# Kernel optimization log

Measured on AMD Instinct MI355X. Metric: run time of the kernel, lower is better.

## Reference

```python
import jax, jax.numpy as jnp
import numpy as np

N, NFEAT, NHID, NCLASS, NLAYERS = 4096, 512, 512, 40, 3
NEG = -9e15


def _adj(key, p=0.01):
    # sparse binary adjacency with self-loops, matching the `adj > 0` masking
    a = (jax.random.uniform(key, (N, N)) < p).astype(jnp.float32)
    return jnp.minimum(a + jnp.eye(N, dtype=jnp.float32), 1.0)


def setup_inputs() -> dict:
    key = jax.random.key(0)
    ks = jax.random.split(key, 16)
    inp = {
        "x": jax.random.normal(ks[0], (N, NFEAT), jnp.float32),
        "adj_att": _adj(ks[1]),
        "adj1": _adj(ks[2]),
        "adj2": _adj(ks[3]),
        "hop_select": jnp.ones((NLAYERS,), jnp.float32),
    }
    s1 = 1.0 / np.sqrt(NFEAT)
    s2 = 1.0 / np.sqrt(NHID)
    for i in range(NLAYERS):
        inp[f"W_fc{i}"] = jax.random.uniform(ks[4 + i], (NFEAT, NHID), jnp.float32, -s1, s1)
        inp[f"b_fc{i}"] = jnp.zeros((NHID,), jnp.float32)
    for i in range(NLAYERS - 1):
        inp[f"W_q{i}"] = jax.random.uniform(ks[7 + 2 * i], (NHID, NHID), jnp.float32, -s2, s2)
        inp[f"b_q{i}"] = jnp.zeros((NHID,), jnp.float32)
        inp[f"W_k{i}"] = jax.random.uniform(ks[8 + 2 * i], (NHID, NHID), jnp.float32, -s2, s2)
        inp[f"b_k{i}"] = jnp.zeros((NHID,), jnp.float32)
    s3 = 1.0 / np.sqrt(NHID * NLAYERS)
    inp["W_cls"] = jax.random.uniform(ks[11], (NHID * NLAYERS, NCLASS), jnp.float32, -s3, s3)
    inp["b_cls"] = jnp.zeros((NCLASS,), jnp.float32)
    return inp


def _gatv3_forward(x, adj_att, adj1, adj2, hop_select,
                   W_fc0, b_fc0, W_fc1, b_fc1, W_fc2, b_fc2,
                   W_q0, b_q0, W_k0, b_k0, W_q1, b_q1, W_k1, b_k1,
                   W_cls, b_cls):
    mask = jax.nn.softmax(hop_select, axis=-1)
    adjs = [None, adj1, adj2]
    fc = [(W_fc0, b_fc0), (W_fc1, b_fc1), (W_fc2, b_fc2)]
    qk = [(W_q0, b_q0, W_k0, b_k0), (W_q1, b_q1, W_k1, b_k1)]
    outs = []
    tmp_1 = None
    for i in range(NLAYERS):
        W, b = fc[i]
        tmp = x @ W + b  # [N, nhid]
        if adjs[i] is not None:
            adj = adjs[i]
            Wq, bq, Wk, bk = qk[i - 1]
            t_att = adj_att @ tmp                      # [N, nhid]
            Q = adj_att @ (t_att @ Wq + bq)            # GCN1 Q, act=None
            K = adj_att @ (t_att @ Wk + bk)            # GCN1 K, act=None
            scores = jnp.where(adj > 0, Q @ K.T, NEG)  # masked QK^T
            att = jax.nn.softmax(scores, axis=-1)
            tmp_1 = jnp.where(adj > 0, att, 0.0)
            tmp = att @ tmp
        # F.normalize(p=2, dim=1) with eps=1e-12 clamp
        nrm = jnp.maximum(jnp.sqrt(jnp.sum(tmp * tmp, axis=1, keepdims=True)), 1e-12)
        outs.append(mask[i] * (tmp / nrm))
    final = jnp.concatenate(outs, axis=1)          # [N, 3*nhid]
    out = jax.nn.relu(final)                       # dropout is identity in eval
    logits = out @ W_cls + b_cls
    return jax.nn.log_softmax(logits, axis=1), tmp_1


def reference(x, adj_att, adj1, adj2, hop_select,
              W_fc0, b_fc0, W_fc1, b_fc1, W_fc2, b_fc2,
              W_q0, b_q0, W_k0, b_k0, W_q1, b_q1, W_k1, b_k1,
              W_cls, b_cls):
    return _gatv3_forward(x, adj_att, adj1, adj2, hop_select,
                          W_fc0, b_fc0, W_fc1, b_fc1, W_fc2, b_fc2,
                          W_q0, b_q0, W_k0, b_k0, W_q1, b_q1, W_k1, b_k1,
                          W_cls, b_cls)
```

## Files before the change

kernel.cpp:

```cpp
#include <hip/hip_runtime.h>
#include <math.h>

#define NN 4096
#define DD 512
#define ELL 128

typedef unsigned long long u64;
typedef __attribute__((ext_vector_type(8))) short short8;
typedef __attribute__((ext_vector_type(8))) unsigned short ushort8;
typedef __attribute__((ext_vector_type(4))) float f32x4;

static __device__ __forceinline__ unsigned short f2bf(float f) {
  unsigned u = __float_as_uint(f);
  unsigned r = (u + 0x7fffu + ((u >> 16) & 1u)) >> 16;
  return (unsigned short)r;
}
static __device__ __forceinline__ float bf2f(unsigned short h) {
  return __uint_as_float(((unsigned)h) << 16);
}

struct Build3 {
  const float *adj0, *adj1, *adj2;
  int *c0, *c1, *c2;
  int *n0, *n1, *n2;
};

__global__ __launch_bounds__(256) void k_build3(Build3 p) {
  const int s = blockIdx.y;
  const float* adj = s == 0 ? p.adj0 : (s == 1 ? p.adj1 : p.adj2);
  int* cols = s == 0 ? p.c0 : (s == 1 ? p.c1 : p.c2);
  int* cnt  = s == 0 ? p.n0 : (s == 1 ? p.n1 : p.n2);
  const int wv = threadIdx.x >> 6;
  const int lane = threadIdx.x & 63;
  const int r = blockIdx.x * 4 + wv;
  const float* row = adj + (size_t)r * NN;
  int* rc = cols + (size_t)r * ELL;
  int base = 0;
  for (int c0 = 0; c0 < NN; c0 += 256) {
    float4 v = *(const float4*)(row + c0 + lane * 4);
    u64 m0 = __ballot(v.x > 0.f);
    u64 m1 = __ballot(v.y > 0.f);
    u64 m2 = __ballot(v.z > 0.f);
    u64 m3 = __ballot(v.w > 0.f);
    u64 below = (1ull << lane) - 1ull;
    int pre = base + __popcll(m0 & below) + __popcll(m1 & below) +
              __popcll(m2 & below) + __popcll(m3 & below);
    int own = 0;
    const int cb = c0 + 4 * lane;
    if (v.x > 0.f) { int id = pre + own; if (id < ELL) rc[id] = cb + 0; own++; }
    if (v.y > 0.f) { int id = pre + own; if (id < ELL) rc[id] = cb + 1; own++; }
    if (v.z > 0.f) { int id = pre + own; if (id < ELL) rc[id] = cb + 2; own++; }
    if (v.w > 0.f) { int id = pre + own; if (id < ELL) rc[id] = cb + 3; own++; }
    base += __popcll(m0) + __popcll(m1) + __popcll(m2) + __popcll(m3);
  }
  if (lane == 0) cnt[r] = base < ELL ? base : ELL;
}

struct SplitE { const float* src; unsigned short* dst; int rows; int bstyle; };
struct Split4 { SplitE e[4]; };

__global__ __launch_bounds__(256) void k_split(Split4 p) {
  SplitE e = p.e[blockIdx.y];
  if (!e.src) return;
  const int oct = blockIdx.x * 256 + threadIdx.x;
  if (oct >= e.rows * 64) return;
  float v[8];
  size_t toff;
  if (!e.bstyle) {
    const int m = oct >> 6, kg = oct & 63;
    const float* sp = e.src + (size_t)m * 512 + kg * 8;
    float4 u0 = *(const float4*)sp;
    float4 u1 = *(const float4*)(sp + 4);
    v[0] = u0.x; v[1] = u0.y; v[2] = u0.z; v[3] = u0.w;
    v[4] = u1.x; v[5] = u1.y; v[6] = u1.z; v[7] = u1.w;
    toff = ((size_t)(m >> 7) * 16 + (kg >> 2)) * 4096 +
           (size_t)((m & 127) >> 4) * 512 + (size_t)(kg & 3) * 128 +
           (size_t)(m & 15) * 8;
  } else {
    const int n = oct & 511, kog = oct >> 9;
    const int k0 = kog * 8;
#pragma unroll
    for (int i = 0; i < 8; i++) v[i] = e.src[(size_t)(k0 + i) * 512 + n];
    toff = ((size_t)(n >> 7) * 16 + (kog >> 2)) * 4096 +
           (size_t)((n & 127) >> 4) * 512 + (size_t)(kog & 3) * 128 +
           (size_t)(n & 15) * 8;
  }
  ushort8 h0, h1, h2;
#pragma unroll
  for (int i = 0; i < 8; i++) {
    float f = v[i];
    unsigned short a0 = f2bf(f);
    float r1 = f - bf2f(a0);
    unsigned short a1 = f2bf(r1);
    float r2 = r1 - bf2f(a1);
    unsigned short a2 = f2bf(r2);
    h0[i] = a0; h1[i] = a1; h2[i] = a2;
  }
  const size_t stride = (size_t)e.rows * 512;
  *(ushort8*)(e.dst + toff) = h0;
  *(ushort8*)(e.dst + stride + toff) = h1;
  *(ushort8*)(e.dst + 2 * stride + toff) = h2;
}

struct ToBf {
  const float *s0, *s1;
  unsigned short *d0, *d1;
};

__global__ __launch_bounds__(256) void k_tobf16(ToBf p) {
  const float* s = blockIdx.y ? p.s1 : p.s0;
  unsigned short* d = blockIdx.y ? p.d1 : p.d0;
  const size_t i = ((size_t)blockIdx.x * 256 + threadIdx.x) * 8;
  float4 a = *(const float4*)(s + i);
  float4 b = *(const float4*)(s + i + 4);
  ushort8 h;
  h[0] = f2bf(a.x); h[1] = f2bf(a.y); h[2] = f2bf(a.z); h[3] = f2bf(a.w);
  h[4] = f2bf(b.x); h[5] = f2bf(b.y); h[6] = f2bf(b.z); h[7] = f2bf(b.w);
  *(ushort8*)(d + i) = h;
}

struct GmP {
  const unsigned short *A0, *A1, *A2;
  const unsigned short *B0, *B1, *B2;
  const float *b0, *b1, *b2;
  float *C0, *C1, *C2;
  size_t sA, sB;
};

#define MMTERM(sa)                                                          \
  _Pragma("unroll")                                                         \
  for (int mi = 0; mi < 4; mi++) {                                          \
    _Pragma("unroll")                                                       \
    for (int ni = 0; ni < 4; ni++)                                          \
      acc[mi][ni] = __builtin_amdgcn_mfma_f32_16x16x32_bf16(                \
          af[sa][mi], bf[ni], acc[mi][ni], 0, 0, 0);                        \
  }

__global__ __launch_bounds__(256) void k_gemm_mfma(GmP p) {
  __shared__ __align__(16) unsigned short Al[3][4096];
  __shared__ __align__(16) unsigned short Bl[3][4096];
  const int tid = threadIdx.x;
  const int mat = blockIdx.y >> 2;
  const int nb = blockIdx.y & 3;
  const int mb = blockIdx.x;
  const unsigned short* A = mat == 0 ? p.A0 : (mat == 1 ? p.A1 : p.A2);
  const unsigned short* B = mat == 0 ? p.B0 : (mat == 1 ? p.B1 : p.B2);
  const float* bias = mat == 0 ? p.b0 : (mat == 1 ? p.b1 : p.b2);
  float* C = mat == 0 ? p.C0 : (mat == 1 ? p.C1 : p.C2);
  const int lane = tid & 63, w = tid >> 6, wr = w >> 1, wc = w & 1;
  const size_t s8A = p.sA >> 3, s8B = p.sB >> 3;

  f32x4 acc[4][4];
#pragma unroll
  for (int mi = 0; mi < 4; mi++)
#pragma unroll
    for (int ni = 0; ni < 4; ni++) acc[mi][ni] = (f32x4){0.f, 0.f, 0.f, 0.f};

  for (int kb = 0; kb < 16; kb++) {
    const short8* ga = (const short8*)(A + ((size_t)mb * 16 + kb) * 4096);
    const short8* gb = (const short8*)(B + ((size_t)nb * 16 + kb) * 4096);
    __syncthreads();
#pragma unroll
    for (int s = 0; s < 3; s++) {
#pragma unroll
      for (int c = 0; c < 2; c++) {
        const int o = tid + c * 256;
        ((short8*)Al[s])[o] = ga[(size_t)s * s8A + o];
        ((short8*)Bl[s])[o] = gb[(size_t)s * s8B + o];
      }
    }
    __syncthreads();
    short8 af[3][4];
#pragma unroll
    for (int s = 0; s < 3; s++)
#pragma unroll
      for (int mi = 0; mi < 4; mi++)
        af[s][mi] = ((const short8*)Al[s])[(wr * 4 + mi) * 64 + lane];
    short8 bf[4];
#pragma unroll
    for (int ni = 0; ni < 4; ni++)
      bf[ni] = ((const short8*)Bl[0])[(wc * 4 + ni) * 64 + lane];
    MMTERM(0) MMTERM(1) MMTERM(2)
#pragma unroll
    for (int ni = 0; ni < 4; ni++)
      bf[ni] = ((const short8*)Bl[1])[(wc * 4 + ni) * 64 + lane];
    MMTERM(0) MMTERM(1)
#pragma unroll
    for (int ni = 0; ni < 4; ni++)
      bf[ni] = ((const short8*)Bl[2])[(wc * 4 + ni) * 64 + lane];
    MMTERM(0)
  }

  const int m0 = mb * 128 + wr * 64;
  const int n0c = nb * 128 + wc * 64 + (lane & 15);
  const int r0 = (lane >> 4) * 4;
#pragma unroll
  for (int mi = 0; mi < 4; mi++) {
#pragma unroll
    for (int ni = 0; ni < 4; ni++) {
      const int col = n0c + ni * 16;
      const float bb = bias ? bias[col] : 0.f;
      f32x4 a = acc[mi][ni];
#pragma unroll
      for (int r = 0; r < 4; r++)
        C[(size_t)(m0 + mi * 16 + r0 + r) * DD + col] = a[r] + bb;
    }
  }
}

struct GemmNT {
  const float *A0, *B0, *A1, *B1;
  float *C0, *C1;
};

__global__ __launch_bounds__(256) void k_gemm_nt(GemmNT p) {
  __shared__ __align__(16) float As[32][68];
  __shared__ __align__(16) float Bs[32][68];
  const int tid = threadIdx.x;
  const int mat = blockIdx.y >> 3;
  const int n0 = (blockIdx.y & 7) * 64;
  const int m0 = blockIdx.x * 64;
  const float* A = mat == 0 ? p.A0 : p.A1;
  const float* B = mat == 0 ? p.B0 : p.B1;
  float* C       = mat == 0 ? p.C0 : p.C1;
  const int tx = tid & 15, ty = tid >> 4;
  const int lr = tid >> 3, lc = (tid & 7) * 4;

  float4 fa[2], fb[2];
#pragma unroll
  for (int q = 0; q < 2; q++) {
    fa[q] = *(const float4*)(A + (size_t)(m0 + lr + 32 * q) * DD + lc);
    fb[q] = *(const float4*)(B + (size_t)(n0 + lr + 32 * q) * DD + lc);
  }
#pragma unroll
  for (int q = 0; q < 2; q++) {
    As[lc + 0][lr + 32 * q] = fa[q].x;
    As[lc + 1][lr + 32 * q] = fa[q].y;
    As[lc + 2][lr + 32 * q] = fa[q].z;
    As[lc + 3][lr + 32 * q] = fa[q].w;
    Bs[lc + 0][lr + 32 * q] = fb[q].x;
    Bs[lc + 1][lr + 32 * q] = fb[q].y;
    Bs[lc + 2][lr + 32 * q] = fb[q].z;
    Bs[lc + 3][lr + 32 * q] = fb[q].w;
  }
  __syncthreads();

  float acc[4][4];
#pragma unroll
  for (int i = 0; i < 4; i++)
#pragma unroll
    for (int j = 0; j < 4; j++) acc[i][j] = 0.f;

  for (int t = 0; t < 16; t++) {
    if (t < 15) {
      const int k0 = (t + 1) * 32;
#pragma unroll
      for (int q = 0; q < 2; q++) {
        fa[q] = *(const float4*)(A + (size_t)(m0 + lr + 32 * q) * DD + k0 + lc);
        fb[q] = *(const float4*)(B + (size_t)(n0 + lr + 32 * q) * DD + k0 + lc);
      }
    }
#pragma unroll
    for (int kk = 0; kk < 32; kk++) {
      float4 a = *(const float4*)&As[kk][ty * 4];
      float4 b = *(const float4*)&Bs[kk][tx * 4];
      float av[4] = {a.x, a.y, a.z, a.w};
      float bv[4] = {b.x, b.y, b.z, b.w};
#pragma unroll
      for (int i = 0; i < 4; i++)
#pragma unroll
        for (int j = 0; j < 4; j++) acc[i][j] = fmaf(av[i], bv[j], acc[i][j]);
    }
    __syncthreads();
    if (t < 15) {
#pragma unroll
      for (int q = 0; q < 2; q++) {
        As[lc + 0][lr + 32 * q] = fa[q].x;
        As[lc + 1][lr + 32 * q] = fa[q].y;
        As[lc + 2][lr + 32 * q] = fa[q].z;
        As[lc + 3][lr + 32 * q] = fa[q].w;
        Bs[lc + 0][lr + 32 * q] = fb[q].x;
        Bs[lc + 1][lr + 32 * q] = fb[q].y;
        Bs[lc + 2][lr + 32 * q] = fb[q].z;
        Bs[lc + 3][lr + 32 * q] = fb[q].w;
      }
      __syncthreads();
    }
  }

#pragma unroll
  for (int i = 0; i < 4; i++) {
    const int m = m0 + ty * 4 + i;
    float4 o = {acc[i][0], acc[i][1], acc[i][2], acc[i][3]};
    *(float4*)(C + (size_t)m * DD + n0 + tx * 4) = o;
  }
}

struct W12P {
  const float *Wq0, *bk0, *Wk0, *bq0;
  const float *Wq1, *bk1, *Wk1, *bq1;
  float *w10, *w20, *w11, *w21, *gam;
};

__global__ __launch_bounds__(256) void k_w12(W12P p) {
  const int l = blockIdx.y;
  const float* Wq = l ? p.Wq1 : p.Wq0;
  const float* bk = l ? p.bk1 : p.bk0;
  const float* Wk = l ? p.Wk1 : p.Wk0;
  const float* bq = l ? p.bq1 : p.bq0;
  float* w1 = l ? p.w11 : p.w10;
  float* w2 = l ? p.w21 : p.w20;
  const int wv = threadIdx.x >> 6, lane = threadIdx.x & 63;
  const int r = blockIdx.x * 4 + wv;
  float s1 = 0.f, s2 = 0.f;
  for (int k = lane; k < DD; k += 64) {
    s1 = fmaf(Wq[(size_t)r * DD + k], bk[k], s1);
    s2 = fmaf(Wk[(size_t)r * DD + k], bq[k], s2);
  }
#pragma unroll
  for (int off = 32; off > 0; off >>= 1) {
    s1 += __shfl_xor(s1, off);
    s2 += __shfl_xor(s2, off);
  }
  if (lane == 0) { w1[r] = s1; w2[r] = s2; }
  if (blockIdx.x == 0 && wv == 0) {
    float g = 0.f;
    for (int k = lane; k < DD; k += 64) g = fmaf(bq[k], bk[k], g);
#pragma unroll
    for (int off = 32; off > 0; off >>= 1) g += __shfl_xor(g, off);
    if (lane == 0) p.gam[l] = g;
  }
}

struct AbP {
  const float *U1, *U2, *w10, *w20, *w11, *w21;
  float *a1, *b1, *a2, *b2;
};

__global__ __launch_bounds__(256) void k_ab(AbP p) {
  const int wv = threadIdx.x >> 6, lane = threadIdx.x & 63;
  const int r = blockIdx.x * 4 + wv;
  const int base = lane * 8;
  float4 wa0 = *(const float4*)(p.w10 + base);
  float4 wa1 = *(const float4*)(p.w10 + base + 4);
  float4 wb0 = *(const float4*)(p.w20 + base);
  float4 wb1 = *(const float4*)(p.w20 + base + 4);
  float4 u0 = *(const float4*)(p.U1 + (size_t)r * DD + base);
  float4 u1 = *(const float4*)(p.U1 + (size_t)r * DD + base + 4);
  float sa = u0.x * wa0.x + u0.y * wa0.y + u0.z * wa0.z + u0.w * wa0.w +
             u1.x * wa1.x + u1.y * wa1.y + u1.z * wa1.z + u1.w * wa1.w;
  float sb = u0.x * wb0.x + u0.y * wb0.y + u0.z * wb0.z + u0.w * wb0.w +
             u1.x * wb1.x + u1.y * wb1.y + u1.z * wb1.z + u1.w * wb1.w;
#pragma unroll
  for (int off = 32; off > 0; off >>= 1) {
    sa += __shfl_xor(sa, off);
    sb += __shfl_xor(sb, off);
  }
  if (lane == 0) { p.a1[r] = sa; p.b1[r] = sb; }
  wa0 = *(const float4*)(p.w11 + base);
  wa1 = *(const float4*)(p.w11 + base + 4);
  wb0 = *(const float4*)(p.w21 + base);
  wb1 = *(const float4*)(p.w21 + base + 4);
  u0 = *(const float4*)(p.U2 + (size_t)r * DD + base);
  u1 = *(const float4*)(p.U2 + (size_t)r * DD + base + 4);
  sa = u0.x * wa0.x + u0.y * wa0.y + u0.z * wa0.z + u0.w * wa0.w +
       u1.x * wa1.x + u1.y * wa1.y + u1.z * wa1.z + u1.w * wa1.w;
  sb = u0.x * wb0.x + u0.y * wb0.y + u0.z * wb0.z + u0.w * wb0.w +
       u1.x * wb1.x + u1.y * wb1.y + u1.z * wb1.z + u1.w * wb1.w;
#pragma unroll
  for (int off = 32; off > 0; off >>= 1) {
    sa += __shfl_xor(sa, off);
    sb += __shfl_xor(sb, off);
  }
  if (lane == 0) { p.a2[r] = sa; p.b2[r] = sb; }
}

struct ScP {
  const int *cols0, *cnts0, *cols1, *cnts1;
  const float *V0, *U0, *al0, *be0;
  const float *V1, *U1, *al1, *be1;
  const float* gam;
  const int* degA;
  float *av0, *av1, *dense;
};

__global__ __launch_bounds__(256) void k_score(ScP p) {
  const int l = blockIdx.y;
  const int* cols = l ? p.cols1 : p.cols0;
  const int* cnts = l ? p.cnts1 : p.cnts0;
  const float* V = l ? p.V1 : p.V0;
  const float* U = l ? p.U1 : p.U0;
  const float* al = l ? p.al1 : p.al0;
  const float* be = l ? p.be1 : p.be0;
  float* av = l ? p.av1 : p.av0;
  float* dense = l ? p.dense : nullptr;
  const int r = blockIdx.x;
  const int t = threadIdx.x;
  const int lane = t & 63, wv = t >> 6;
  const int cnt = cnts[r];
  __shared__ int scol[ELL];
  __shared__ float ssc[ELL];
  if (t < ELL) scol[t] = (t < cnt) ? cols[(size_t)r * ELL + t] : 0;
  if (dense) {
    float4 z = {0.f, 0.f, 0.f, 0.f};
    float4* drow = (float4*)(dense + (size_t)r * NN);
#pragma unroll
    for (int q = 0; q < 4; q++) drow[t + 256 * q] = z;
  }
  __syncthreads();
  const float g = p.gam[l];
  const float dr = (float)p.degA[r];
  const float ar = al[r];
  const float* Vr = V + (size_t)r * DD + lane * 8;
  float4 q0 = *(const float4*)Vr;
  float4 q1 = *(const float4*)(Vr + 4);
  for (int k = wv; k < cnt; k += 4) {
    const int c = scol[k];
    const float* Uc = U + (size_t)c * DD + lane * 8;
    float4 k0 = *(const float4*)Uc;
    float4 k1 = *(const float4*)(Uc + 4);
    float s = q0.x * k0.x + q0.y * k0.y + q0.z * k0.z + q0.w * k0.w +
              q1.x * k1.x + q1.y * k1.y + q1.z * k1.z + q1.w * k1.w;
#pragma unroll
    for (int off = 32; off > 0; off >>= 1) s += __shfl_xor(s, off);
    if (lane == 0) {
      const float dc = (float)p.degA[c];
      ssc[k] = s + dc * ar + dr * be[c] + dr * dc * g;
    }
  }
  __syncthreads();
  if (wv == 0) {
    float v0 = (lane < cnt) ? ssc[lane] : -INFINITY;
    float v1 = (lane + 64 < cnt) ? ssc[lane + 64] : -INFINITY;
    float mx = fmaxf(v0, v1);
#pragma unroll
    for (int off = 32; off > 0; off >>= 1) mx = fmaxf(mx, __shfl_xor(mx, off));
    float e0 = (lane < cnt) ? expf(v0 - mx) : 0.f;
    float e1 = (lane + 64 < cnt) ? expf(v1 - mx) : 0.f;
    float sm = e0 + e1;
#pragma unroll
    for (int off = 32; off > 0; off >>= 1) sm += __shfl_xor(sm, off);
    float inv = 1.f / sm;
    if (lane < cnt) ssc[lane] = e0 * inv;
    if (lane + 64 < cnt) ssc[lane + 64] = e1 * inv;
  }
  __syncthreads();
  if (t < cnt) {
    const float v = ssc[t];
    av[(size_t)r * ELL + t] = v;
    if (dense) dense[(size_t)r * NN + scol[t]] = v;
  }
}

struct PvP {
  const int *cols0, *cnts0, *cols1, *cnts1;
  const float *av0, *av1;
  const unsigned short *T0, *T1;
  float *out0, *out1;
};

__global__ __launch_bounds__(256) void k_pv(PvP p) {
  const int l = blockIdx.y;
  const int* cols = l ? p.cols1 : p.cols0;
  const int* cnts = l ? p.cnts1 : p.cnts0;
  const float* av = l ? p.av1 : p.av0;
  const unsigned short* Tb = l ? p.T1 : p.T0;
  float* out = l ? p.out1 : p.out0;
  const int hr = threadIdx.x >> 7;
  const int j = threadIdx.x & 127;
  const int row = blockIdx.x * 2 + hr;
  __shared__ int scol[2][ELL];
  __shared__ float sval[2][ELL];
  const int cnt = cnts[row];
  scol[hr][j] = (j < cnt) ? cols[(size_t)row * ELL + j] : 0;
  sval[hr][j] = (j < cnt) ? av[(size_t)row * ELL + j] : 0.f;
  __syncthreads();
  float a0 = 0.f, a1 = 0.f, a2 = 0.f, a3 = 0.f;
#pragma unroll 4
  for (int k = 0; k < cnt; k++) {
    const float v = sval[hr][k];
    const uint2 u = *(const uint2*)(Tb + (size_t)scol[hr][k] * DD + j * 4);
    a0 = fmaf(v, __uint_as_float(u.x << 16), a0);
    a1 = fmaf(v, __uint_as_float(u.x & 0xffff0000u), a1);
    a2 = fmaf(v, __uint_as_float(u.y << 16), a2);
    a3 = fmaf(v, __uint_as_float(u.y & 0xffff0000u), a3);
  }
  float4 o = {a0, a1, a2, a3};
  *(float4*)(out + (size_t)row * DD + j * 4) = o;
}

struct SpF {
  const int *colsA, *cntsA, *colsB, *cntsB;
  const float *BA, *BB;
  float *CA, *CB;
};

__global__ __launch_bounds__(256) void k_spmm_f4(SpF p) {
  const int mat = blockIdx.y;
  const int* cols = mat ? p.colsB : p.colsA;
  const int* cnts = mat ? p.cntsB : p.cntsA;
  const float* B = mat ? p.BB : p.BA;
  float* C = mat ? p.CB : p.CA;
  const int hr = threadIdx.x >> 7;
  const int j = threadIdx.x & 127;
  const int row = blockIdx.x * 2 + hr;
  __shared__ int scol[2][ELL];
  const int cnt = cnts[row];
  scol[hr][j] = (j < cnt) ? cols[(size_t)row * ELL + j] : 0;
  __syncthreads();
  float4 acc = {0.f, 0.f, 0.f, 0.f};
#pragma unroll 4
  for (int k = 0; k < cnt; k++) {
    float4 b = *(const float4*)(B + (size_t)scol[hr][k] * DD + j * 4);
    acc.x += b.x; acc.y += b.y; acc.z += b.z; acc.w += b.w;
  }
  *(float4*)(C + (size_t)row * DD + j * 4) = acc;
}

__global__ __launch_bounds__(256) void k_norm_cls(const float* __restrict__ T0,
                                                  const float* __restrict__ T1,
                                                  const float* __restrict__ T2,
                                                  const float* __restrict__ hop,
                                                  const float* __restrict__ Wc,
                                                  const float* __restrict__ bc,
                                                  float* __restrict__ out) {
  const int r = blockIdx.x;
  const int t = threadIdx.x;
  const int lane = t & 63, wv = t >> 6;
  __shared__ __align__(16) float srow[1536];
  __shared__ float red[4];
  __shared__ float pr[6][40];
  float h0 = hop[0], h1 = hop[1], h2 = hop[2];
  float hm = fmaxf(h0, fmaxf(h1, h2));
  float e0 = expf(h0 - hm), e1 = expf(h1 - hm), e2 = expf(h2 - hm);
  float minv = 1.f / (e0 + e1 + e2);
  float mask[3] = {e0 * minv, e1 * minv, e2 * minv};
  const float* Ts[3] = {T0, T1, T2};
#pragma unroll
  for (int s = 0; s < 3; s++) {
    float x0 = Ts[s][(size_t)r * DD + t];
    float x1 = Ts[s][(size_t)r * DD + t + 256];
    float ss = x0 * x0 + x1 * x1;
#pragma unroll
    for (int off = 32; off > 0; off >>= 1) ss += __shfl_xor(ss, off);
    if (lane == 0) red[wv] = ss;
    __syncthreads();
    float tot = red[0] + red[1] + red[2] + red[3];
    float nrm = fmaxf(sqrtf(tot), 1e-12f);
    float sc = mask[s] / nrm;
    srow[s * DD + t] = fmaxf(x0 * sc, 0.f);
    srow[s * DD + t + 256] = fmaxf(x1 * sc, 0.f);
    __syncthreads();
  }
  float part = 0.f;
  const int col = t % 40, seg = t / 40;
  if (seg < 6) {
    const float* w = Wc + col;
#pragma unroll 4
    for (int k = seg * 256; k < seg * 256 + 256; k++)
      part = fmaf(srow[k], w[(size_t)k * 40], part);
    pr[seg][col] = part;
  }
  __syncthreads();
  if (t < 64) {
    float lg = -INFINITY;
    if (t < 40) {
      lg = bc[t];
#pragma unroll
      for (int s6 = 0; s6 < 6; s6++) lg += pr[s6][t];
    }
    float mx = lg;
#pragma unroll
    for (int off = 32; off > 0; off >>= 1) mx = fmaxf(mx, __shfl_xor(mx, off));
    float ex = (t < 40) ? expf(lg - mx) : 0.f;
    float sm = ex;
#pragma unroll
    for (int off = 32; off > 0; off >>= 1) sm += __shfl_xor(sm, off);
    float ls = logf(sm);
    if (t < 40) out[(size_t)r * 40 + t] = lg - mx - ls;
  }
}

extern "C" void kernel_launch(void* const* d_in, const int* in_sizes, int n_in,
                              void* d_out, int out_size, void* d_ws, size_t ws_size,
                              hipStream_t stream) {
  (void)in_sizes; (void)n_in; (void)out_size; (void)ws_size;
  const float* x    = (const float*)d_in[0];
  const float* adjA = (const float*)d_in[1];
  const float* adj1 = (const float*)d_in[2];
  const float* adj2 = (const float*)d_in[3];
  const float* hop  = (const float*)d_in[4];
  const float* Wfc0 = (const float*)d_in[5];  const float* bfc0 = (const float*)d_in[6];
  const float* Wfc1 = (const float*)d_in[7];  const float* bfc1 = (const float*)d_in[8];
  const float* Wfc2 = (const float*)d_in[9];  const float* bfc2 = (const float*)d_in[10];
  const float* Wq0  = (const float*)d_in[11]; const float* bq0  = (const float*)d_in[12];
  const float* Wk0  = (const float*)d_in[13]; const float* bk0  = (const float*)d_in[14];
  const float* Wq1  = (const float*)d_in[15]; const float* bq1  = (const float*)d_in[16];
  const float* Wk1  = (const float*)d_in[17]; const float* bk1  = (const float*)d_in[18];
  const float* Wc   = (const float*)d_in[19]; const float* bc   = (const float*)d_in[20];

  float* ws = (float*)d_ws;
  const size_t MD = (size_t)NN * DD;
  const size_t WD = (size_t)DD * DD;
  float* TMP0 = ws + 0 * MD;
  float* TMP1 = ws + 1 * MD;
  float* TMP2 = ws + 2 * MD;
  float* S3   = ws + 3 * MD;
  float* S4   = ws + 4 * MD;
  float* U1   = ws + 5 * MD;
  float* U2   = ws + 6 * MD;
  float* M1   = ws + 7 * MD;
  float* M2   = M1 + WD;
  float* w10 = M2 + WD;
  float* w20 = w10 + DD;
  float* w11 = w20 + DD;
  float* w21 = w11 + DD;
  float* gam = w21 + DD;
  float* AL1 = gam + 4;
  float* BE1 = AL1 + NN;
  float* AL2 = BE1 + NN;
  float* BE2 = AL2 + NN;
  int* ELLA = (int*)(BE2 + NN);
  int* ELL1 = ELLA + (size_t)NN * ELL;
  int* ELL2 = ELL1 + (size_t)NN * ELL;
  int* CNTA = ELL2 + (size_t)NN * ELL;
  int* CNT1 = CNTA + NN;
  int* CNT2 = CNT1 + NN;
  unsigned short* Tb1 = (unsigned short*)(CNT2 + NN);
  unsigned short* Tb2 = Tb1 + MD;
  float* ATTV1 = TMP1;
  float* ATTV2 = TMP2;

  float* outLog = (float*)d_out;
  float* outAtt = outLog + (size_t)NN * 40;
  unsigned short* xb   = (unsigned short*)outAtt;
  unsigned short* wfcb = xb + 3 * MD;
  unsigned short* Ub1  = wfcb + 9 * WD;
  unsigned short* Ub2  = Ub1 + 3 * MD;
  unsigned short* Mb1  = Ub2 + 3 * MD;
  unsigned short* Mb2  = Mb1 + 3 * WD;

  Build3 pb{adjA, adj1, adj2, ELLA, ELL1, ELL2, CNTA, CNT1, CNT2};
  k_build3<<<dim3(NN / 4, 3), 256, 0, stream>>>(pb);

  W12P pw{Wq0, bk0, Wk0, bq0, Wq1, bk1, Wk1, bq1, w10, w20, w11, w21, gam};
  k_w12<<<dim3(DD / 4, 2), 256, 0, stream>>>(pw);

  Split4 sp1{{{x, xb, NN, 0},
              {Wfc0, wfcb + 0 * 3 * WD, DD, 1},
              {Wfc1, wfcb + 1 * 3 * WD, DD, 1},
              {Wfc2, wfcb + 2 * 3 * WD, DD, 1}}};
  k_split<<<dim3(1024, 4), 256, 0, stream>>>(sp1);

  GmP pf{xb, xb, xb,
         wfcb + 0 * 3 * WD, wfcb + 1 * 3 * WD, wfcb + 2 * 3 * WD,
         bfc0, bfc1, bfc2, TMP0, TMP1, TMP2, MD, WD};
  k_gemm_mfma<<<dim3(32, 12), 256, 0, stream>>>(pf);

  GemmNT pm{Wq0, Wk0, Wq1, Wk1, M1, M2};
  k_gemm_nt<<<dim3(8, 16), 256, 0, stream>>>(pm);

  ToBf tb{TMP1, TMP2, Tb1, Tb2};
  k_tobf16<<<dim3(1024, 2), 256, 0, stream>>>(tb);

  SpF s1{ELLA, CNTA, ELLA, CNTA, TMP1, TMP2, S3, S4};
  k_spmm_f4<<<dim3(NN / 2, 2), 256, 0, stream>>>(s1);
  SpF s2{ELLA, CNTA, ELLA, CNTA, S3, S4, U1, U2};
  k_spmm_f4<<<dim3(NN / 2, 2), 256, 0, stream>>>(s2);

  Split4 sp2{{{U1, Ub1, NN, 0},
              {U2, Ub2, NN, 0},
              {M1, Mb1, DD, 1},
              {M2, Mb2, DD, 1}}};
  k_split<<<dim3(1024, 4), 256, 0, stream>>>(sp2);

  GmP pv{Ub1, Ub2, nullptr, Mb1, Mb2, nullptr,
         nullptr, nullptr, nullptr, S3, S4, nullptr, MD, WD};
  k_gemm_mfma<<<dim3(32, 8), 256, 0, stream>>>(pv);

  AbP pab{U1, U2, w10, w20, w11, w21, AL1, BE1, AL2, BE2};
  k_ab<<<NN / 4, 256, 0, stream>>>(pab);

  ScP sc{ELL1, CNT1, ELL2, CNT2,
         S3, U1, AL1, BE1,
         S4, U2, AL2, BE2,
         gam, CNTA, ATTV1, ATTV2, outAtt};
  k_score<<<dim3(NN, 2), 256, 0, stream>>>(sc);

  PvP pp{ELL1, CNT1, ELL2, CNT2, ATTV1, ATTV2, Tb1, Tb2, S3, S4};
  k_pv<<<dim3(NN / 2, 2), 256, 0, stream>>>(pp);

  k_norm_cls<<<NN, 256, 0, stream>>>(TMP0, S3, S4, hop, Wc, bc, outLog);
}
```

Measured before the change: 430.5 us.

## Build ELL adjacency lists with one block per row and prefix scan

The adjacency-to-ELL conversion now assigns a whole 256-thread block to each row instead of one wavefront per row looping over 16 chunks. Each thread loads 16 contiguous floats at once, builds a bitmask, and a wave shuffle scan plus a shared-memory cross-wave sum gives each thread its write offset. This aims to raise memory-level parallelism when streaming the three dense 4096x4096 adjacency matrices. The cost is more blocks, a __syncthreads, and a serial per-thread bit loop for the writes.

```diff
diff --git a/kernel.cpp b/kernel.cpp
--- a/kernel.cpp
+++ b/kernel.cpp
@@ -30,30 +30,52 @@
   const float* adj = s == 0 ? p.adj0 : (s == 1 ? p.adj1 : p.adj2);
   int* cols = s == 0 ? p.c0 : (s == 1 ? p.c1 : p.c2);
   int* cnt  = s == 0 ? p.n0 : (s == 1 ? p.n1 : p.n2);
-  const int wv = threadIdx.x >> 6;
-  const int lane = threadIdx.x & 63;
-  const int r = blockIdx.x * 4 + wv;
-  const float* row = adj + (size_t)r * NN;
+  const int r = blockIdx.x;
+  const int t = threadIdx.x;
+  const int lane = t & 63, wv = t >> 6;
+  const float* row = adj + (size_t)r * NN + t * 16;
   int* rc = cols + (size_t)r * ELL;
+
+  float4 v0 = *(const float4*)(row + 0);
+  float4 v1 = *(const float4*)(row + 4);
+  float4 v2 = *(const float4*)(row + 8);
+  float4 v3 = *(const float4*)(row + 12);
+  unsigned mask = 0;
+  mask |= (v0.x > 0.f) << 0;  mask |= (v0.y > 0.f) << 1;
+  mask |= (v0.z > 0.f) << 2;  mask |= (v0.w > 0.f) << 3;
+  mask |= (v1.x > 0.f) << 4;  mask |= (v1.y > 0.f) << 5;
+  mask |= (v1.z > 0.f) << 6;  mask |= (v1.w > 0.f) << 7;
+  mask |= (v2.x > 0.f) << 8;  mask |= (v2.y > 0.f) << 9;
+  mask |= (v2.z > 0.f) << 10; mask |= (v2.w > 0.f) << 11;
+  mask |= (v3.x > 0.f) << 12; mask |= (v3.y > 0.f) << 13;
+  mask |= (v3.z > 0.f) << 14; mask |= (v3.w > 0.f) << 15;
+  const int mycnt = __popc(mask);
+
+  int incl = mycnt;
+#pragma unroll
+  for (int off = 1; off < 64; off <<= 1) {
+    int n = __shfl_up(incl, off);
+    if (lane >= off) incl += n;
+  }
+  __shared__ int wsum[4];
+  if (lane == 63) wsum[wv] = incl;
+  __syncthreads();
   int base = 0;
-  for (int c0 = 0; c0 < NN; c0 += 256) {
-    float4 v = *(const float4*)(row + c0 + lane * 4);
-    u64 m0 = __ballot(v.x > 0.f);
-    u64 m1 = __ballot(v.y > 0.f);
-    u64 m2 = __ballot(v.z > 0.f);
-    u64 m3 = __ballot(v.w > 0.f);
-    u64 below = (1ull << lane) - 1ull;
-    int pre = base + __popcll(m0 & below) + __popcll(m1 & below) +
-              __popcll(m2 & below) + __popcll(m3 & below);
-    int own = 0;
-    const int cb = c0 + 4 * lane;
-    if (v.x > 0.f) { int id = pre + own; if (id < ELL) rc[id] = cb + 0; own++; }
-    if (v.y > 0.f) { int id = pre + own; if (id < ELL) rc[id] = cb + 1; own++; }
-    if (v.z > 0.f) { int id = pre + own; if (id < ELL) rc[id] = cb + 2; own++; }
-    if (v.w > 0.f) { int id = pre + own; if (id < ELL) rc[id] = cb + 3; own++; }
-    base += __popcll(m0) + __popcll(m1) + __popcll(m2) + __popcll(m3);
-  }
-  if (lane == 0) cnt[r] = base < ELL ? base : ELL;
+#pragma unroll
+  for (int w = 0; w < 4; w++)
+    if (w < wv) base += wsum[w];
+  int off = base + incl - mycnt;
+  unsigned m = mask;
+  while (m) {
+    const int b = __ffs(m) - 1;
+    if (off < ELL) rc[off] = t * 16 + b;
+    off++;
+    m &= m - 1;
+  }
+  if (t == 255) {
+    const int tot = base + incl;
+    cnt[r] = tot < ELL ? tot : ELL;
+  }
 }
 
 struct SplitE { const float* src; unsigned short* dst; int rows; int bstyle; };
@@ -641,7 +663,7 @@
   unsigned short* Mb2  = Mb1 + 3 * WD;
 
   Build3 pb{adjA, adj1, adj2, ELLA, ELL1, ELL2, CNTA, CNT1, CNT2};
-  k_build3<<<dim3(NN / 4, 3), 256, 0, stream>>>(pb);
+  k_build3<<<dim3(NN, 3), 256, 0, stream>>>(pb);
 
   W12P pw{Wq0, bk0, Wk0, bq0, Wq1, bk1, Wk1, bq1, w10, w20, w11, w21, gam};
   k_w12<<<dim3(DD / 4, 2), 256, 0, stream>>>(pw);
```

Result: no change. 424.2 us (-1.5%).
